# Performance work log

Hardware: AMD Instinct MI355X
Metric: run time of the kernel (lower is better)

Reference implementation:

```python
import jax, jax.numpy as jnp
import numpy as np

EPS = 0.1
MAX_ITER = 10
SIGMA = 0.1
NEG_INF = -1e8


def gaussian_position_filter(in_size, out_size, dtype):
    a = jnp.arange(0.0, in_size, dtype=dtype)[:, None] / in_size
    b = jnp.arange(0.0, out_size, dtype=dtype)[None, :] / out_size
    return jnp.exp(-(((a - b) / SIGMA) ** 2))[None]


def log_sinkhorn(K, mask, max_iter):
    # K: n x in_size x out_size (already scaled by 1/eps); mask: n x in_size bool
    n, in_size, out_size = K.shape
    dt = K.dtype
    loga = jnp.log((out_size / mask.sum(1, keepdims=True)).astype(dt))  # n x 1

    def neg_lse(u, v, axis):
        Z = K + u[:, :, None] + v[:, None, :]
        return -jax.nn.logsumexp(Z, axis=axis)

    def body(carry, _):
        u, v = carry
        u = loga + neg_lse(u, v, -1)           # row update: n x in_size
        u = jnp.where(mask, u, jnp.asarray(NEG_INF, dt))
        v = neg_lse(u, v, 1)                   # col update: n x out_size
        return (u, v), None

    u0 = jnp.zeros((n, in_size), dt)
    v0 = jnp.zeros((n, out_size), dt)
    (u, v), _ = jax.lax.scan(body, (u0, v0), None, length=max_iter)
    return jnp.exp(K + u[:, :, None] + v[:, None, :])  # transport plan T


def setup_inputs() -> dict:
    key = jax.random.key(0)
    k1, k2, k3 = jax.random.split(key, 3)
    B, S, O, D = 16, 4096, 512, 128
    return {
        "input": jax.random.normal(k1, (B, S, D), jnp.float32),
        "target": jax.random.normal(k2, (B, O, D), jnp.float32),
        "iou_cost": jax.random.uniform(k3, (B, S, O), jnp.float32),
        "mask": jnp.ones((B, S), jnp.bool_),
    }


def reference(input, target, iou_cost, mask):
    # input: B x S x D, target: B x O x D, iou_cost: B x S x O, mask: B x S
    B, S, D = input.shape
    O = target.shape[1]
    pf = gaussian_position_filter(S, O, input.dtype)
    K = jnp.einsum('bsd,bod->bso', input, target) - iou_cost  # similarity minus IoU cost
    K = pf * K / EPS
    T = pf * log_sinkhorn(K, mask, MAX_ITER) * S              # B x S x O
    # output: B x (out_size*heads) x in_size, heads=1
    return jnp.transpose(T, (0, 2, 1)).reshape(B, O, S)
```

## Files before the change

### kernel.cpp

```cpp
#include <hip/hip_runtime.h>
#include <hip/hip_bf16.h>

#define B_ 16
#define S_ 4096
#define O_ 512
#define D_ 128
#define NEG_INF_ -1e8f
#define MAX_ITER_ 10
#define YST 513

typedef __attribute__((ext_vector_type(8))) short short8;
typedef __attribute__((ext_vector_type(4))) float floatx4;
typedef __attribute__((ext_vector_type(4))) unsigned short ushort4v;

__device__ inline unsigned short f32_to_bf16_rne(float x) {
    union { float f; unsigned int u; } c; c.f = x;
    unsigned int u = c.u;
    unsigned int r = (u + 0x7FFFu + ((u >> 16) & 1u)) >> 16;
    return (unsigned short)r;
}
__device__ inline float bf16_bits_to_f32(unsigned short h) {
    union { unsigned int u; float f; } c; c.u = ((unsigned int)h) << 16;
    return c.f;
}

__global__ void init_kernel(const int* __restrict__ mask,
                            float* __restrict__ u, float* __restrict__ v,
                            float* __restrict__ loga) {
    __shared__ int sc[256];
    int b = blockIdx.x, t = threadIdx.x;
    int c = 0;
    for (int k = t; k < S_; k += 256) c += (mask[(size_t)b * S_ + k] != 0);
    sc[t] = c; __syncthreads();
    for (int st = 128; st > 0; st >>= 1) { if (t < st) sc[t] += sc[t + st]; __syncthreads(); }
    if (t == 0) loga[b] = logf((float)O_ / (float)sc[0]);
    for (int k = t; k < S_; k += 256) u[(size_t)b * S_ + k] = 0.f;
    for (int k = t; k < O_; k += 256) v[b * O_ + k] = 0.f;
}

__global__ __launch_bounds__(256) void split_kernel(const float* __restrict__ srcA,
                                                    unsigned short* __restrict__ hiA,
                                                    unsigned short* __restrict__ loA, int n4A,
                                                    const float* __restrict__ srcB,
                                                    unsigned short* __restrict__ hiB,
                                                    unsigned short* __restrict__ loB, int n4B) {
    int i = blockIdx.x * 256 + threadIdx.x;
    const float* src; unsigned short* hi; unsigned short* lo;
    if (i < n4A) { src = srcA; hi = hiA; lo = loA; }
    else if (i < n4A + n4B) { i -= n4A; src = srcB; hi = hiB; lo = loB; }
    else return;
    float4 x = ((const float4*)src)[i];
    float xs[4] = {x.x, x.y, x.z, x.w};
    ushort4v h, l;
#pragma unroll
    for (int j = 0; j < 4; ++j) {
        unsigned short hh = f32_to_bf16_rne(xs[j]);
        float rem = xs[j] - bf16_bits_to_f32(hh);
        h[j] = hh; l[j] = f32_to_bf16_rne(rem);
    }
    ((ushort4v*)hi)[i] = h;
    ((ushort4v*)lo)[i] = l;
}

__global__ __launch_bounds__(256) void gemm_nat(const unsigned short* __restrict__ in_hi,
                                                const unsigned short* __restrict__ in_lo,
                                                const unsigned short* __restrict__ tg_hi,
                                                const unsigned short* __restrict__ tg_lo,
                                                const float* __restrict__ iou,
                                                float* __restrict__ K) {
    int b = blockIdx.z;
    int s0 = blockIdx.x * 256;
    int o0 = blockIdx.y * 64;
    int t = threadIdx.x, wid = t >> 6, lane = t & 63, fr = lane & 15, kg = lane >> 4;

    const unsigned short* ih = in_hi + ((size_t)b * S_ + s0 + wid * 64 + fr) * D_;
    const unsigned short* il = in_lo + ((size_t)b * S_ + s0 + wid * 64 + fr) * D_;
    const unsigned short* th = tg_hi + ((size_t)b * O_ + o0 + fr) * D_;
    const unsigned short* tl = tg_lo + ((size_t)b * O_ + o0 + fr) * D_;

    floatx4 acc[4][4];
#pragma unroll
    for (int i = 0; i < 4; ++i)
#pragma unroll
        for (int j = 0; j < 4; ++j) acc[i][j] = (floatx4){0.f, 0.f, 0.f, 0.f};

#pragma unroll
    for (int kb = 0; kb < 4; ++kb) {
        int ko = kb * 32 + kg * 8;
        short8 T_h[4], T_l[4];
#pragma unroll
        for (int j = 0; j < 4; ++j) {
            T_h[j] = *(const short8*)(th + (size_t)j * 16 * D_ + ko);
            T_l[j] = *(const short8*)(tl + (size_t)j * 16 * D_ + ko);
        }
#pragma unroll
        for (int i = 0; i < 4; ++i) {
            short8 I_h = *(const short8*)(ih + (size_t)i * 16 * D_ + ko);
            short8 I_l = *(const short8*)(il + (size_t)i * 16 * D_ + ko);
#pragma unroll
            for (int j = 0; j < 4; ++j) {
                acc[i][j] = __builtin_amdgcn_mfma_f32_16x16x32_bf16(T_l[j], I_h, acc[i][j], 0, 0, 0);
                acc[i][j] = __builtin_amdgcn_mfma_f32_16x16x32_bf16(T_h[j], I_l, acc[i][j], 0, 0, 0);
                acc[i][j] = __builtin_amdgcn_mfma_f32_16x16x32_bf16(T_h[j], I_h, acc[i][j], 0, 0, 0);
            }
        }
    }

#pragma unroll
    for (int i = 0; i < 4; ++i) {
        int s = s0 + wid * 64 + i * 16 + fr;
        float sn = (float)s * (1.0f / S_);
        size_t rowb = ((size_t)b * S_ + s) * O_;
#pragma unroll
        for (int j = 0; j < 4; ++j) {
            int ob = o0 + j * 16 + kg * 4;
            float4 iv = *(const float4*)(iou + rowb + ob);
            float ivs[4] = {iv.x, iv.y, iv.z, iv.w};
            float tmp[4];
#pragma unroll
            for (int r = 0; r < 4; ++r) {
                float d = sn - (float)(ob + r) * (1.0f / O_);
                float pf = __expf(-100.0f * d * d);
                tmp[r] = pf * (acc[i][j][r] - ivs[r]) * 10.0f;
            }
            float4 q; q.x = tmp[0]; q.y = tmp[1]; q.z = tmp[2]; q.w = tmp[3];
            *(float4*)(K + rowb + ob) = q;
        }
    }
}

template <int FIRST>
__global__ __launch_bounds__(256) void sink_iter(const float* __restrict__ K,
                                                 const float* __restrict__ vin,
                                                 float* __restrict__ u,
                                                 float2* __restrict__ colma,
                                                 const int* __restrict__ mask,
                                                 const float* __restrict__ loga) {
    __shared__ float sv[O_];
    __shared__ float sy[16 * YST];
    int b = blockIdx.y;
    int t = threadIdx.x, fr = t & 15, sl = t >> 4;
    if (!FIRST) {
        for (int i = t; i < O_; i += 256) sv[i] = vin[b * O_ + i];
        __syncthreads();
    }
    int sbase = blockIdx.x * 64;
    float lg = loga[b];
    float Mc0 = -INFINITY, Ac0 = 0.f, Mc1 = -INFINITY, Ac1 = 0.f;

    float bufA[32], bufB[32];
    auto loadK = [&](float (&dst)[32], int tau) {
        const float* krow = K + ((size_t)b * S_ + sbase + tau * 16 + sl) * O_ + fr * 4;
#pragma unroll
        for (int k = 0; k < 8; ++k) {
            float4 q = *(const float4*)(krow + k * 64);
            dst[k * 4 + 0] = q.x; dst[k * 4 + 1] = q.y;
            dst[k * 4 + 2] = q.z; dst[k * 4 + 3] = q.w;
        }
    };
    auto process = [&](float (&cur)[32], float (&nxt)[32], int tau, bool pre) {
        int s = sbase + tau * 16 + sl;
        size_t srow = (size_t)b * S_ + s;
        float uold = FIRST ? 0.f : u[srow];
        int mk = mask[srow];
        if (pre) loadK(nxt, tau + 1);

        float xv[32];
        if (FIRST) {
#pragma unroll
            for (int i = 0; i < 32; ++i) xv[i] = cur[i];
        } else {
#pragma unroll
            for (int k = 0; k < 8; ++k) {
                float4 vvq = *(const float4*)&sv[fr * 4 + k * 64];
                xv[k * 4 + 0] = cur[k * 4 + 0] + uold + vvq.x;
                xv[k * 4 + 1] = cur[k * 4 + 1] + uold + vvq.y;
                xv[k * 4 + 2] = cur[k * 4 + 2] + uold + vvq.z;
                xv[k * 4 + 3] = cur[k * 4 + 3] + uold + vvq.w;
            }
        }
        float M = -INFINITY;
#pragma unroll
        for (int i = 0; i < 32; ++i) M = fmaxf(M, xv[i]);
#pragma unroll
        for (int off = 1; off < 16; off <<= 1) M = fmaxf(M, __shfl_xor(M, off));
        float a = 0.f;
#pragma unroll
        for (int i = 0; i < 32; ++i) a += __expf(xv[i] - M);
#pragma unroll
        for (int off = 1; off < 16; off <<= 1) a += __shfl_xor(a, off);
        float unew = lg - (M + logf(a));
        if (!mk) unew = NEG_INF_;
        if (fr == 0) u[srow] = unew;

        float c = unew - uold;
#pragma unroll
        for (int k = 0; k < 8; ++k) {
            float4 q;
            q.x = xv[k * 4 + 0] + c; q.y = xv[k * 4 + 1] + c;
            q.z = xv[k * 4 + 2] + c; q.w = xv[k * 4 + 3] + c;
            *(float4*)&sy[sl * YST + fr * 4 + k * 64] = q;
        }
        __syncthreads();
#pragma unroll
        for (int h = 0; h < 2; ++h) {
            int o = t + h * 256;
            float q[16];
            float m = -INFINITY;
#pragma unroll
            for (int r = 0; r < 16; ++r) { q[r] = sy[r * YST + o]; m = fmaxf(m, q[r]); }
            float aa = 0.f;
#pragma unroll
            for (int r = 0; r < 16; ++r) aa += __expf(q[r] - m);
            float Mo = h ? Mc1 : Mc0, Ao = h ? Ac1 : Ac0;
            float nm = fmaxf(Mo, m);
            Ao = Ao * __expf(Mo - nm) + aa * __expf(m - nm);
            if (h) { Mc1 = nm; Ac1 = Ao; } else { Mc0 = nm; Ac0 = Ao; }
        }
        __syncthreads();
    };
    loadK(bufA, 0);
    process(bufA, bufB, 0, true);
    process(bufB, bufA, 1, true);
    process(bufA, bufB, 2, true);
    process(bufB, bufA, 3, false);

    float2* cout = colma + ((size_t)b * 64 + blockIdx.x) * O_;
    {
        float2 r0; r0.x = Mc0; r0.y = Ac0;
        cout[t] = r0;
        float2 r1; r1.x = Mc1; r1.y = Ac1;
        cout[t + 256] = r1;
    }
}

__global__ __launch_bounds__(256) void finalize_v(const float2* __restrict__ colma,
                                                  float* __restrict__ v) {
    __shared__ float sm[4][64], sa[4][64];
    int b = blockIdx.y;
    int ol = threadIdx.x & 63, cg = threadIdx.x >> 6;
    int o = blockIdx.x * 64 + ol;
    const float2* cp = colma + (size_t)b * 64 * O_ + o;
    float M = -INFINITY, A = 0.f;
#pragma unroll 4
    for (int i = 0; i < 16; ++i) {
        float2 q = cp[(size_t)(cg * 16 + i) * O_];
        float nm = fmaxf(M, q.x);
        A = A * __expf(M - nm) + q.y * __expf(q.x - nm);
        M = nm;
    }
    sm[cg][ol] = M; sa[cg][ol] = A;
    __syncthreads();
    if (threadIdx.x < 64) {
        M = sm[0][ol]; A = sa[0][ol];
#pragma unroll
        for (int i = 1; i < 4; ++i) {
            float mi = sm[i][ol], ai = sa[i][ol];
            float nm = fmaxf(M, mi);
            A = A * __expf(M - nm) + ai * __expf(mi - nm);
            M = nm;
        }
        v[b * O_ + o] = -(M + logf(A));
    }
}

__global__ __launch_bounds__(256) void final_tr(const float* __restrict__ K,
                                                const float* __restrict__ u,
                                                const float* __restrict__ v,
                                                float* __restrict__ out) {
    __shared__ float tile[64][65];
    __shared__ float su[64], svv[64];
    int b = blockIdx.z;
    int s0 = blockIdx.x * 64, o0 = blockIdx.y * 64;
    int t = threadIdx.x, fr = t & 15, rg = t >> 4;
    if (t < 64) su[t] = u[(size_t)b * S_ + s0 + t];
    else if (t < 128) svv[t - 64] = v[b * O_ + o0 + t - 64];
    __syncthreads();
#pragma unroll
    for (int p = 0; p < 4; ++p) {
        int sl = p * 16 + rg;
        int s = s0 + sl;
        float4 x = *(const float4*)(K + ((size_t)b * S_ + s) * O_ + o0 + fr * 4);
        float us = su[sl];
        float sn = (float)s * (1.0f / S_);
        float xs[4] = {x.x, x.y, x.z, x.w};
#pragma unroll
        for (int c = 0; c < 4; ++c) {
            int ol = fr * 4 + c;
            float d = sn - (float)(o0 + ol) * (1.0f / O_);
            tile[ol][sl] = 4096.0f * __expf(xs[c] + us + svv[ol] - 100.0f * d * d);
        }
    }
    __syncthreads();
#pragma unroll
    for (int p = 0; p < 4; ++p) {
        int ol = p * 16 + rg;
        float4 y;
        y.x = tile[ol][fr * 4 + 0];
        y.y = tile[ol][fr * 4 + 1];
        y.z = tile[ol][fr * 4 + 2];
        y.w = tile[ol][fr * 4 + 3];
        *(float4*)(out + ((size_t)b * O_ + o0 + ol) * S_ + s0 + fr * 4) = y;
    }
}


__global__ __launch_bounds__(256) void gemm_kt2(const unsigned short* __restrict__ in_hi,
                                                const unsigned short* __restrict__ in_lo,
                                                const unsigned short* __restrict__ tg_hi,
                                                const unsigned short* __restrict__ tg_lo,
                                                const float* __restrict__ iou,
                                                float* __restrict__ KT) {
    __shared__ float siou[64 * 65];
    int b = blockIdx.z;
    int s0 = blockIdx.x * 64;
    int o0 = blockIdx.y * 64;
    int t = threadIdx.x;
    {
        const float* ir = iou + ((size_t)b * S_ + s0 + (t >> 2)) * O_ + o0 + (t & 3) * 16;
        float4 q0 = ((const float4*)ir)[0];
        float4 q1 = ((const float4*)ir)[1];
        float4 q2 = ((const float4*)ir)[2];
        float4 q3 = ((const float4*)ir)[3];
        float* dst = &siou[(t >> 2) * 65 + (t & 3) * 16];
        dst[0]=q0.x; dst[1]=q0.y; dst[2]=q0.z; dst[3]=q0.w;
        dst[4]=q1.x; dst[5]=q1.y; dst[6]=q1.z; dst[7]=q1.w;
        dst[8]=q2.x; dst[9]=q2.y; dst[10]=q2.z; dst[11]=q2.w;
        dst[12]=q3.x; dst[13]=q3.y; dst[14]=q3.z; dst[15]=q3.w;
    }
    int w = t >> 6, lane = t & 63, fr = lane & 15, kg = lane >> 4;
    const unsigned short* ta_hi = tg_hi + ((size_t)b * O_ + o0 + w * 16 + fr) * D_;
    const unsigned short* ta_lo = tg_lo + ((size_t)b * O_ + o0 + w * 16 + fr) * D_;
    const unsigned short* ib_hi = in_hi + ((size_t)b * S_ + s0 + fr) * D_;
    const unsigned short* ib_lo = in_lo + ((size_t)b * S_ + s0 + fr) * D_;
    floatx4 acc[4];
#pragma unroll
    for (int st = 0; st < 4; ++st) acc[st] = (floatx4){0.f, 0.f, 0.f, 0.f};
#pragma unroll
    for (int kb = 0; kb < 4; ++kb) {
        int ko = kb * 32 + kg * 8;
        short8 ah = *(const short8*)(ta_hi + ko);
        short8 al2 = *(const short8*)(ta_lo + ko);
#pragma unroll
        for (int st = 0; st < 4; ++st) {
            short8 bh2 = *(const short8*)(ib_hi + (size_t)st * 16 * D_ + ko);
            short8 bl2 = *(const short8*)(ib_lo + (size_t)st * 16 * D_ + ko);
            acc[st] = __builtin_amdgcn_mfma_f32_16x16x32_bf16(al2, bh2, acc[st], 0, 0, 0);
            acc[st] = __builtin_amdgcn_mfma_f32_16x16x32_bf16(ah, bl2, acc[st], 0, 0, 0);
            acc[st] = __builtin_amdgcn_mfma_f32_16x16x32_bf16(ah, bh2, acc[st], 0, 0, 0);
        }
    }
    __syncthreads();
#pragma unroll
    for (int st = 0; st < 4; ++st) {
        int s = s0 + st * 16 + fr;
        float ds = (float)s * (1.0f / S_);
#pragma unroll
        for (int r = 0; r < 4; ++r) {
            int o = o0 + w * 16 + kg * 4 + r;
            float d = ds - (float)o * (1.0f / O_);
            float pf = __expf(-100.0f * d * d);
            float iouv = siou[(st * 16 + fr) * 65 + (w * 16 + kg * 4 + r)];
            KT[((size_t)b * O_ + o) * S_ + s] = pf * (acc[st][r] - iouv) * 10.0f;
        }
    }
}

__global__ __launch_bounds__(256) void row_update2(const float* __restrict__ KT,
                                                   const float* __restrict__ v,
                                                   float* __restrict__ u,
                                                   const int* __restrict__ mask,
                                                   const float* __restrict__ loga) {
    __shared__ float sv[O_];
    __shared__ float lm[4][128], la[4][128];
    int b = blockIdx.y;
    int s0 = blockIdx.x * 128;
    int t = threadIdx.x, lane = t & 63, w = t >> 6;
    for (int i = t; i < O_; i += 256) sv[i] = v[b * O_ + i];
    __syncthreads();
    const float* kt = KT + (size_t)b * O_ * S_ + s0 + lane * 2;
    float m0 = -INFINITY, m1 = -INFINITY, a0 = 0.f, a1 = 0.f;
    int ob = w * 128;
#pragma unroll 8
    for (int i = 0; i < 128; ++i) {
        int o = ob + i;
        float2 x2 = *(const float2*)(kt + (size_t)o * S_);
        float vo = sv[o];
        float x0 = x2.x + vo, x1 = x2.y + vo;
        if (x0 > m0) { a0 = a0 * __expf(m0 - x0) + 1.f; m0 = x0; } else a0 += __expf(x0 - m0);
        if (x1 > m1) { a1 = a1 * __expf(m1 - x1) + 1.f; m1 = x1; } else a1 += __expf(x1 - m1);
    }
    lm[w][lane * 2] = m0;     la[w][lane * 2] = a0;
    lm[w][lane * 2 + 1] = m1; la[w][lane * 2 + 1] = a1;
    __syncthreads();
    if (t < 128) {
        float M = lm[0][t], A = la[0][t];
#pragma unroll
        for (int i = 1; i < 4; ++i) {
            float mi = lm[i][t], ai = la[i][t];
            float nm = fmaxf(M, mi);
            A = A * __expf(M - nm) + ai * __expf(mi - nm);
            M = nm;
        }
        float lse = M + logf(A);
        size_t si = (size_t)b * S_ + s0 + t;
        u[si] = mask[si] ? (loga[b] - u[si] - lse) : NEG_INF_;
    }
}

template <int FIN>
__global__ __launch_bounds__(256) void col_update2(float* __restrict__ KT,
                                                   const float* __restrict__ u,
                                                   float* __restrict__ v) {
    __shared__ float red[8];
    int b = blockIdx.y, o = blockIdx.x;
    int t = threadIdx.x;
    float* kt = KT + ((size_t)b * O_ + o) * S_;
    const float* ub = u + (size_t)b * S_;
    float vold = v[b * O_ + o];
    float xs[16];
    float m = -INFINITY, a = 0.f;
#pragma unroll
    for (int k = 0; k < 4; ++k) {
        int s = k * 1024 + t * 4;
        float4 kx = *(const float4*)(kt + s);
        float4 ux = *(const float4*)(ub + s);
        float x0 = kx.x + ux.x, x1 = kx.y + ux.y, x2 = kx.z + ux.z, x3 = kx.w + ux.w;
        if (FIN) { xs[k*4] = x0; xs[k*4+1] = x1; xs[k*4+2] = x2; xs[k*4+3] = x3; }
        float cm = fmaxf(fmaxf(x0, x1), fmaxf(x2, x3));
        float nm = fmaxf(m, cm);
        a = a * __expf(m - nm) + __expf(x0 - nm) + __expf(x1 - nm)
                               + __expf(x2 - nm) + __expf(x3 - nm);
        m = nm;
    }
#pragma unroll
    for (int off = 1; off < 64; off <<= 1) {
        float mo = __shfl_xor(m, off), ao = __shfl_xor(a, off);
        float nm = fmaxf(m, mo);
        a = a * __expf(m - nm) + ao * __expf(mo - nm);
        m = nm;
    }
    int w = t >> 6;
    if ((t & 63) == 0) { red[w * 2] = m; red[w * 2 + 1] = a; }
    __syncthreads();
    float M = red[0], A = red[1];
#pragma unroll
    for (int i = 1; i < 4; ++i) {
        float mi = red[i * 2], ai = red[i * 2 + 1];
        float nm = fmaxf(M, mi);
        A = A * __expf(M - nm) + ai * __expf(mi - nm);
        M = nm;
    }
    float lse = M + logf(A);
    float vn = -vold - lse;
    if (t == 0) v[b * O_ + o] = vn;
    if (FIN) {
        float oo = (float)o * (1.0f / O_);
#pragma unroll
        for (int k = 0; k < 4; ++k) {
            int s = k * 1024 + t * 4;
            float4 r;
            float rr[4];
#pragma unroll
            for (int j = 0; j < 4; ++j) {
                float d = (float)(s + j) * (1.0f / S_) - oo;
                rr[j] = 4096.0f * __expf(xs[k * 4 + j] + vn - 100.0f * d * d);
            }
            r.x = rr[0]; r.y = rr[1]; r.z = rr[2]; r.w = rr[3];
            *(float4*)(kt + s) = r;
        }
    }
}


extern "C" void kernel_launch(void* const* d_in, const int* in_sizes, int n_in,
                              void* d_out, int out_size, void* d_ws, size_t ws_size,
                              hipStream_t stream) {
    const float* input  = (const float*)d_in[0];
    const float* target = (const float*)d_in[1];
    const float* iou    = (const float*)d_in[2];
    const int*   mask   = (const int*)d_in[3];
    float* out = (float*)d_out;
    float* wsf = (float*)d_ws;

    const size_t N_IN = (size_t)B_ * S_ * D_;
    const size_t N_TG = (size_t)B_ * O_ * D_;
    const size_t NK   = (size_t)B_ * S_ * O_;

    float* u    = wsf;
    float* v    = u + (size_t)B_ * S_;
    float* loga = v + (size_t)B_ * O_;

    float* Knat = loga + 16;
    float* region = Knat + NK;
    unsigned short* f_in_hi = (unsigned short*)region;
    unsigned short* f_in_lo = f_in_hi + N_IN;
    unsigned short* f_tg_hi = f_in_lo + N_IN;
    unsigned short* f_tg_lo = f_tg_hi + N_TG;
    float2* colma = (float2*)region;
    size_t need_fast = (size_t)((char*)(f_tg_lo + N_TG) - (char*)d_ws);

    unsigned short* m_in_hi = (unsigned short*)(loga + 16);
    unsigned short* m_in_lo = m_in_hi + N_IN;
    unsigned short* m_tg_hi = m_in_lo + N_IN;
    unsigned short* m_tg_lo = m_tg_hi + N_TG;
    size_t need_mid = (size_t)((char*)(m_tg_lo + N_TG) - (char*)d_ws);

    init_kernel<<<B_, 256, 0, stream>>>(mask, u, v, loga);

    if (ws_size >= need_fast) {
        int n4A = (int)(N_IN / 4), n4B = (int)(N_TG / 4);
        split_kernel<<<(n4A + n4B + 255) / 256, 256, 0, stream>>>(
            input, f_in_hi, f_in_lo, n4A, target, f_tg_hi, f_tg_lo, n4B);
        gemm_nat<<<dim3(S_ / 256, O_ / 64, B_), 256, 0, stream>>>(f_in_hi, f_in_lo, f_tg_hi, f_tg_lo, iou, Knat);
        for (int it = 0; it < MAX_ITER_; ++it) {
            if (it == 0)
                sink_iter<1><<<dim3(S_ / 64, B_), 256, 0, stream>>>(Knat, v, u, colma, mask, loga);
            else
                sink_iter<0><<<dim3(S_ / 64, B_), 256, 0, stream>>>(Knat, v, u, colma, mask, loga);
            finalize_v<<<dim3(O_ / 64, B_), 256, 0, stream>>>(colma, v);
        }
        final_tr<<<dim3(S_ / 64, O_ / 64, B_), 256, 0, stream>>>(Knat, u, v, out);
    } else if (ws_size >= need_mid) {
        int n4A = (int)(N_IN / 4), n4B = (int)(N_TG / 4);
        split_kernel<<<(n4A + n4B + 255) / 256, 256, 0, stream>>>(
            input, m_in_hi, m_in_lo, n4A, target, m_tg_hi, m_tg_lo, n4B);
        gemm_kt2<<<dim3(S_ / 64, O_ / 64, B_), 256, 0, stream>>>(m_in_hi, m_in_lo, m_tg_hi, m_tg_lo, iou, out);
        for (int it = 0; it < MAX_ITER_; ++it) {
            row_update2<<<dim3(S_ / 128, B_), 256, 0, stream>>>(out, v, u, mask, loga);
            if (it < MAX_ITER_ - 1)
                col_update2<0><<<dim3(O_, B_), 256, 0, stream>>>(out, u, v);
            else
                col_update2<1><<<dim3(O_, B_), 256, 0, stream>>>(out, u, v);
        }
    }
}
```

Measured before the change: 512.0 us.

## Store shifted log-kernel in fp16 after first Sinkhorn iteration to halve K traffic

After the first iteration, K+u1 is written once as an fp16 matrix. Later iterations and the final transpose read this half-size buffer and add the u delta instead of re-reading the fp32 K. This halves the memory traffic of the nine later sweeps over the 32M-element matrix. The cost is precision: fp16 keeps about 11 bits of mantissa on values that can be large after scaling by 1/eps, and it overflows to -inf where K+u is very negative, which is why reads clamp to NEG_INF. The path needs more workspace and only runs when ws_size is large enough; otherwise it falls back to the old path.

After: 487.5 us (median of 2 runs). -4.8%, faster.

```diff
diff --git a/kernel.cpp b/kernel.cpp
--- a/kernel.cpp
+++ b/kernel.cpp
@@ -12,6 +12,7 @@
 typedef __attribute__((ext_vector_type(8))) short short8;
 typedef __attribute__((ext_vector_type(4))) float floatx4;
 typedef __attribute__((ext_vector_type(4))) unsigned short ushort4v;
+typedef __attribute__((ext_vector_type(4))) _Float16 half4v;
 
 __device__ inline unsigned short f32_to_bf16_rne(float x) {
     union { float f; unsigned int u; } c; c.f = x;
@@ -129,6 +130,236 @@
     }
 }
 
+
+__global__ __launch_bounds__(256) void sink_first_z(const float* __restrict__ K,
+                                                    float* __restrict__ u,
+                                                    float* __restrict__ u1c,
+                                                    _Float16* __restrict__ zh,
+                                                    float2* __restrict__ colma,
+                                                    const int* __restrict__ mask,
+                                                    const float* __restrict__ loga) {
+    __shared__ float sy[16 * YST];
+    int b = blockIdx.y;
+    int t = threadIdx.x, fr = t & 15, sl = t >> 4;
+    int sbase = blockIdx.x * 64;
+    float lg = loga[b];
+    float Mc0 = -INFINITY, Ac0 = 0.f, Mc1 = -INFINITY, Ac1 = 0.f;
+
+    float bufA[32], bufB[32];
+    auto loadK = [&](float (&dst)[32], int tau) {
+        const float* krow = K + ((size_t)b * S_ + sbase + tau * 16 + sl) * O_ + fr * 4;
+#pragma unroll
+        for (int k = 0; k < 8; ++k) {
+            float4 q = *(const float4*)(krow + k * 64);
+            dst[k * 4 + 0] = q.x; dst[k * 4 + 1] = q.y;
+            dst[k * 4 + 2] = q.z; dst[k * 4 + 3] = q.w;
+        }
+    };
+    auto process = [&](float (&cur)[32], float (&nxt)[32], int tau, bool pre) {
+        int s = sbase + tau * 16 + sl;
+        size_t srow = (size_t)b * S_ + s;
+        int mk = mask[srow];
+        if (pre) loadK(nxt, tau + 1);
+
+        float M = -INFINITY;
+#pragma unroll
+        for (int i = 0; i < 32; ++i) M = fmaxf(M, cur[i]);
+#pragma unroll
+        for (int off = 1; off < 16; off <<= 1) M = fmaxf(M, __shfl_xor(M, off));
+        float a = 0.f;
+#pragma unroll
+        for (int i = 0; i < 32; ++i) a += __expf(cur[i] - M);
+#pragma unroll
+        for (int off = 1; off < 16; off <<= 1) a += __shfl_xor(a, off);
+        float unew = lg - (M + logf(a));
+        if (!mk) unew = NEG_INF_;
+        if (fr == 0) { u[srow] = unew; u1c[srow] = unew; }
+
+        float c = unew;
+        _Float16* zw = zh + srow * O_ + fr * 4;
+#pragma unroll
+        for (int k = 0; k < 8; ++k) {
+            float y0 = cur[k * 4 + 0] + c, y1 = cur[k * 4 + 1] + c;
+            float y2 = cur[k * 4 + 2] + c, y3 = cur[k * 4 + 3] + c;
+            float4 q; q.x = y0; q.y = y1; q.z = y2; q.w = y3;
+            *(float4*)&sy[sl * YST + fr * 4 + k * 64] = q;
+            half4v hq;
+            hq[0] = (_Float16)y0; hq[1] = (_Float16)y1;
+            hq[2] = (_Float16)y2; hq[3] = (_Float16)y3;
+            *(half4v*)(zw + k * 64) = hq;
+        }
+        __syncthreads();
+#pragma unroll
+        for (int h = 0; h < 2; ++h) {
+            int o = t + h * 256;
+            float q[16];
+            float m = -INFINITY;
+#pragma unroll
+            for (int r = 0; r < 16; ++r) { q[r] = sy[r * YST + o]; m = fmaxf(m, q[r]); }
+            float aa = 0.f;
+#pragma unroll
+            for (int r = 0; r < 16; ++r) aa += __expf(q[r] - m);
+            float Mo = h ? Mc1 : Mc0, Ao = h ? Ac1 : Ac0;
+            float nm = fmaxf(Mo, m);
+            Ao = Ao * __expf(Mo - nm) + aa * __expf(m - nm);
+            if (h) { Mc1 = nm; Ac1 = Ao; } else { Mc0 = nm; Ac0 = Ao; }
+        }
+        __syncthreads();
+    };
+    loadK(bufA, 0);
+    process(bufA, bufB, 0, true);
+    process(bufB, bufA, 1, true);
+    process(bufA, bufB, 2, true);
+    process(bufB, bufA, 3, false);
+
+    float2* cout = colma + ((size_t)b * 64 + blockIdx.x) * O_;
+    {
+        float2 r0; r0.x = Mc0; r0.y = Ac0; cout[t] = r0;
+        float2 r1; r1.x = Mc1; r1.y = Ac1; cout[t + 256] = r1;
+    }
+}
+
+__global__ __launch_bounds__(256) void sink_late(const _Float16* __restrict__ zh,
+                                                 const float* __restrict__ vin,
+                                                 float* __restrict__ u,
+                                                 const float* __restrict__ u1c,
+                                                 float2* __restrict__ colma,
+                                                 const int* __restrict__ mask,
+                                                 const float* __restrict__ loga) {
+    __shared__ float sv[O_];
+    __shared__ float sy[16 * YST];
+    int b = blockIdx.y;
+    int t = threadIdx.x, fr = t & 15, sl = t >> 4;
+    for (int i = t; i < O_; i += 256) sv[i] = vin[b * O_ + i];
+    __syncthreads();
+    int sbase = blockIdx.x * 64;
+    float lg = loga[b];
+    float Mc0 = -INFINITY, Ac0 = 0.f, Mc1 = -INFINITY, Ac1 = 0.f;
+
+    float bufA[32], bufB[32];
+    auto loadZ = [&](float (&dst)[32], int tau) {
+        const _Float16* zrow = zh + ((size_t)b * S_ + sbase + tau * 16 + sl) * O_ + fr * 4;
+#pragma unroll
+        for (int k = 0; k < 8; ++k) {
+            half4v q = *(const half4v*)(zrow + k * 64);
+            dst[k * 4 + 0] = fmaxf((float)q[0], NEG_INF_);
+            dst[k * 4 + 1] = fmaxf((float)q[1], NEG_INF_);
+            dst[k * 4 + 2] = fmaxf((float)q[2], NEG_INF_);
+            dst[k * 4 + 3] = fmaxf((float)q[3], NEG_INF_);
+        }
+    };
+    auto process = [&](float (&cur)[32], float (&nxt)[32], int tau, bool pre) {
+        int s = sbase + tau * 16 + sl;
+        size_t srow = (size_t)b * S_ + s;
+        float uold = u[srow];
+        float du = uold - u1c[srow];
+        int mk = mask[srow];
+        if (pre) loadZ(nxt, tau + 1);
+
+        float xv[32];
+#pragma unroll
+        for (int k = 0; k < 8; ++k) {
+            float4 vvq = *(const float4*)&sv[fr * 4 + k * 64];
+            xv[k * 4 + 0] = cur[k * 4 + 0] + du + vvq.x;
+            xv[k * 4 + 1] = cur[k * 4 + 1] + du + vvq.y;
+            xv[k * 4 + 2] = cur[k * 4 + 2] + du + vvq.z;
+            xv[k * 4 + 3] = cur[k * 4 + 3] + du + vvq.w;
+        }
+        float M = -INFINITY;
+#pragma unroll
+        for (int i = 0; i < 32; ++i) M = fmaxf(M, xv[i]);
+#pragma unroll
+        for (int off = 1; off < 16; off <<= 1) M = fmaxf(M, __shfl_xor(M, off));
+        float a = 0.f;
+#pragma unroll
+        for (int i = 0; i < 32; ++i) a += __expf(xv[i] - M);
+#pragma unroll
+        for (int off = 1; off < 16; off <<= 1) a += __shfl_xor(a, off);
+        float unew = lg - (M + logf(a));
+        if (!mk) unew = NEG_INF_;
+        if (fr == 0) u[srow] = unew;
+
+        float c = unew - uold;
+#pragma unroll
+        for (int k = 0; k < 8; ++k) {
+            float4 q;
+            q.x = xv[k * 4 + 0] + c; q.y = xv[k * 4 + 1] + c;
+            q.z = xv[k * 4 + 2] + c; q.w = xv[k * 4 + 3] + c;
+            *(float4*)&sy[sl * YST + fr * 4 + k * 64] = q;
+        }
+        __syncthreads();
+#pragma unroll
+        for (int h = 0; h < 2; ++h) {
+            int o = t + h * 256;
+            float q[16];
+            float m = -INFINITY;
+#pragma unroll
+            for (int r = 0; r < 16; ++r) { q[r] = sy[r * YST + o]; m = fmaxf(m, q[r]); }
+            float aa = 0.f;
+#pragma unroll
+            for (int r = 0; r < 16; ++r) aa += __expf(q[r] - m);
+            float Mo = h ? Mc1 : Mc0, Ao = h ? Ac1 : Ac0;
+            float nm = fmaxf(Mo, m);
+            Ao = Ao * __expf(Mo - nm) + aa * __expf(m - nm);
+            if (h) { Mc1 = nm; Ac1 = Ao; } else { Mc0 = nm; Ac0 = Ao; }
+        }
+        __syncthreads();
+    };
+    loadZ(bufA, 0);
+    process(bufA, bufB, 0, true);
+    process(bufB, bufA, 1, true);
+    process(bufA, bufB, 2, true);
+    process(bufB, bufA, 3, false);
+
+    float2* cout = colma + ((size_t)b * 64 + blockIdx.x) * O_;
+    {
+        float2 r0; r0.x = Mc0; r0.y = Ac0; cout[t] = r0;
+        float2 r1; r1.x = Mc1; r1.y = Ac1; cout[t + 256] = r1;
+    }
+}
+
+__global__ __launch_bounds__(256) void final_tr_z(const _Float16* __restrict__ zh,
+                                                  const float* __restrict__ u,
+                                                  const float* __restrict__ u1c,
+                                                  const float* __restrict__ v,
+                                                  float* __restrict__ out) {
+    __shared__ float tile[64][65];
+    __shared__ float sdu[64], svv[64];
+    int b = blockIdx.z;
+    int s0 = blockIdx.x * 64, o0 = blockIdx.y * 64;
+    int t = threadIdx.x, fr = t & 15, rg = t >> 4;
+    if (t < 64) sdu[t] = u[(size_t)b * S_ + s0 + t] - u1c[(size_t)b * S_ + s0 + t];
+    else if (t < 128) svv[t - 64] = v[b * O_ + o0 + t - 64];
+    __syncthreads();
+#pragma unroll
+    for (int p = 0; p < 4; ++p) {
+        int sl = p * 16 + rg;
+        int s = s0 + sl;
+        half4v hx = *(const half4v*)(zh + ((size_t)b * S_ + s) * O_ + o0 + fr * 4);
+        float du = sdu[sl];
+        float sn = (float)s * (1.0f / S_);
+#pragma unroll
+        for (int c = 0; c < 4; ++c) {
+            int ol = fr * 4 + c;
+            float zf = fmaxf((float)hx[c], NEG_INF_);
+            float d = sn - (float)(o0 + ol) * (1.0f / O_);
+            tile[ol][sl] = 4096.0f * __expf(zf + du + svv[ol] - 100.0f * d * d);
+        }
+    }
+    __syncthreads();
+#pragma unroll
+    for (int p = 0; p < 4; ++p) {
+        int ol = p * 16 + rg;
+        float4 y;
+        y.x = tile[ol][fr * 4 + 0];
+        y.y = tile[ol][fr * 4 + 1];
+        y.z = tile[ol][fr * 4 + 2];
+        y.w = tile[ol][fr * 4 + 3];
+        *(float4*)(out + ((size_t)b * O_ + o0 + ol) * S_ + s0 + fr * 4) = y;
+    }
+}
+
+
 template <int FIRST>
 __global__ __launch_bounds__(256) void sink_iter(const float* __restrict__ K,
                                                  const float* __restrict__ vin,
@@ -227,10 +458,8 @@
 
     float2* cout = colma + ((size_t)b * 64 + blockIdx.x) * O_;
     {
-        float2 r0; r0.x = Mc0; r0.y = Ac0;
-        cout[t] = r0;
-        float2 r1; r1.x = Mc1; r1.y = Ac1;
-        cout[t + 256] = r1;
+        float2 r0; r0.x = Mc0; r0.y = Ac0; cout[t] = r0;
+        float2 r1; r1.x = Mc1; r1.y = Ac1; cout[t + 256] = r1;
     }
 }
 
@@ -490,15 +719,20 @@
     float* u    = wsf;
     float* v    = u + (size_t)B_ * S_;
     float* loga = v + (size_t)B_ * O_;
-
-    float* Knat = loga + 16;
-    float* region = Knat + NK;
+    float* u1c  = loga + 16;
+    float* Knat = u1c + (size_t)B_ * S_;
+    char*  region = (char*)(Knat + NK);
+
     unsigned short* f_in_hi = (unsigned short*)region;
     unsigned short* f_in_lo = f_in_hi + N_IN;
     unsigned short* f_tg_hi = f_in_lo + N_IN;
     unsigned short* f_tg_lo = f_tg_hi + N_TG;
+    size_t need_B = (size_t)((char*)(f_tg_lo + N_TG) - (char*)d_ws);
+
     float2* colma = (float2*)region;
-    size_t need_fast = (size_t)((char*)(f_tg_lo + N_TG) - (char*)d_ws);
+    _Float16* zh = (_Float16*)(colma + (size_t)B_ * 64 * O_);
+    size_t need_A = (size_t)((char*)(zh + NK) - (char*)d_ws);
+    if (need_A < need_B) need_A = need_B;
 
     unsigned short* m_in_hi = (unsigned short*)(loga + 16);
     unsigned short* m_in_lo = m_in_hi + N_IN;
@@ -507,9 +741,20 @@
     size_t need_mid = (size_t)((char*)(m_tg_lo + N_TG) - (char*)d_ws);
 
     init_kernel<<<B_, 256, 0, stream>>>(mask, u, v, loga);
-
-    if (ws_size >= need_fast) {
-        int n4A = (int)(N_IN / 4), n4B = (int)(N_TG / 4);
+    int n4A = (int)(N_IN / 4), n4B = (int)(N_TG / 4);
+
+    if (ws_size >= need_A) {
+        split_kernel<<<(n4A + n4B + 255) / 256, 256, 0, stream>>>(
+            input, f_in_hi, f_in_lo, n4A, target, f_tg_hi, f_tg_lo, n4B);
+        gemm_nat<<<dim3(S_ / 256, O_ / 64, B_), 256, 0, stream>>>(f_in_hi, f_in_lo, f_tg_hi, f_tg_lo, iou, Knat);
+        sink_first_z<<<dim3(S_ / 64, B_), 256, 0, stream>>>(Knat, u, u1c, zh, colma, mask, loga);
+        finalize_v<<<dim3(O_ / 64, B_), 256, 0, stream>>>(colma, v);
+        for (int it = 1; it < MAX_ITER_; ++it) {
+            sink_late<<<dim3(S_ / 64, B_), 256, 0, stream>>>(zh, v, u, u1c, colma, mask, loga);
+            finalize_v<<<dim3(O_ / 64, B_), 256, 0, stream>>>(colma, v);
+        }
+        final_tr_z<<<dim3(S_ / 64, O_ / 64, B_), 256, 0, stream>>>(zh, u, u1c, v, out);
+    } else if (ws_size >= need_B) {
         split_kernel<<<(n4A + n4B + 255) / 256, 256, 0, stream>>>(
             input, f_in_hi, f_in_lo, n4A, target, f_tg_hi, f_tg_lo, n4B);
         gemm_nat<<<dim3(S_ / 256, O_ / 64, B_), 256, 0, stream>>>(f_in_hi, f_in_lo, f_tg_hi, f_tg_lo, iou, Knat);
@@ -522,7 +767,6 @@
         }
         final_tr<<<dim3(S_ / 64, O_ / 64, B_), 256, 0, stream>>>(Knat, u, v, out);
     } else if (ws_size >= need_mid) {
-        int n4A = (int)(N_IN / 4), n4B = (int)(N_TG / 4);
         split_kernel<<<(n4A + n4B + 255) / 256, 256, 0, stream>>>(
             input, m_in_hi, m_in_lo, n4A, target, m_tg_hi, m_tg_lo, n4B);
         gemm_kt2<<<dim3(S_ / 64, O_ / 64, B_), 256, 0, stream>>>(m_in_hi, m_in_lo, m_tg_hi, m_tg_lo, iou, out);
```
